# Kernel tuning notes

Hardware: AMD Instinct MI355X
Metric: run time of the kernel (lower is better)

## Reference

```python
import jax, jax.numpy as jnp
import numpy as np

C = 256
POOL = 4

def setup_inputs() -> dict:
    key = jax.random.key(0)
    ks = jax.random.split(key, 8)
    B, H, W = 4, 256, 256
    d = C // 8
    x = jax.random.normal(ks[0], (B, C, H, W), dtype=jnp.float32)
    # 1x1 conv weights stored as [out, in] matrices (kernel_size=1)
    s = 1.0 / np.sqrt(C)
    Wq = jax.random.uniform(ks[1], (d, C), jnp.float32, -s, s)
    bq = jax.random.uniform(ks[2], (d,), jnp.float32, -s, s)
    Wk = jax.random.uniform(ks[3], (d, C), jnp.float32, -s, s)
    bk = jax.random.uniform(ks[4], (d,), jnp.float32, -s, s)
    Wv = jax.random.uniform(ks[5], (C, C), jnp.float32, -s, s)
    bv = jax.random.uniform(ks[6], (C,), jnp.float32, -s, s)
    gamma = jax.random.normal(ks[7], (1,), jnp.float32) * 0.1
    return {"x": x, "Wq": Wq, "bq": bq, "Wk": Wk, "bk": bk,
            "Wv": Wv, "bv": bv, "gamma": gamma}


def reference(x, Wq, bq, Wk, bk, Wv, bv, gamma):
    B, Cc, H, W = x.shape
    Hp, Wp = H // POOL, W // POOL
    # AvgPool2d(kernel=4, stride=4)
    xp = x.reshape(B, Cc, Hp, POOL, Wp, POOL).mean(axis=(3, 5))  # [B,C,Hp,Wp]
    xf = xp.reshape(B, Cc, Hp * Wp)                              # [B,C,N]
    # 1x1 convs == channel matmuls
    q = jnp.einsum('dc,bcn->bdn', Wq, xf) + bq[None, :, None]    # [B,d,N]
    k = jnp.einsum('dc,bcn->bdn', Wk, xf) + bk[None, :, None]    # [B,d,N]
    v = jnp.einsum('ec,bcn->ben', Wv, xf) + bv[None, :, None]    # [B,C,N]
    # energy[b,n,m] = q[:, :, n] . k[:, :, m]
    energy = jnp.einsum('bdn,bdm->bnm', q, k)                    # [B,N,N]
    attn = jax.nn.softmax(energy, axis=-1)
    # out = v @ attn^T  -> out[b,c,n] = sum_m v[b,c,m] * attn[b,n,m]
    out = jnp.einsum('bcm,bnm->bcn', v, attn)                    # [B,C,N]
    out = out.reshape(B, Cc, Hp, Wp)
    # bilinear upsample, half-pixel centers (align_corners=False)
    up = jax.image.resize(out, (B, Cc, H, W), method='bilinear')
    return gamma[0] * up + x
```

## Files before the change

### kernel.cpp

```cpp
#include <hip/hip_runtime.h>

#define B_ 4
#define C_ 256
#define N_ 4096
#define D_ 32

typedef __bf16 bf16;
typedef __bf16 bf16x4 __attribute__((ext_vector_type(4)));
typedef __bf16 bf16x8 __attribute__((ext_vector_type(8)));
typedef float f32x4 __attribute__((ext_vector_type(4)));

__global__ __launch_bounds__(256) void k_prep(
    const float* __restrict__ Wq, const float* __restrict__ bq,
    const float* __restrict__ Wk, const float* __restrict__ bk,
    const float* __restrict__ Wv, const float* __restrict__ bv,
    bf16* __restrict__ wt, float* __restrict__ bias) {
  int r = blockIdx.x, t = threadIdx.x;
  const float* src; float bval;
  if (r < 32)      { src = Wq + (r << 8);        bval = bq[r]; }
  else if (r < 64) { src = Wk + ((r - 32) << 8); bval = bk[r - 32]; }
  else             { src = Wv + ((r - 64) << 8); bval = bv[r - 64]; }
  wt[(r << 8) + t] = (bf16)src[t];
  if (t == 0) bias[r] = bval;
}

__global__ __launch_bounds__(1024) void k_fused(const float* __restrict__ x,
    const bf16* __restrict__ wt, const float* __restrict__ bias,
    bf16* __restrict__ qt, bf16* __restrict__ kt, bf16* __restrict__ v) {
  __shared__ bf16 xsb[64][264];
  int tid = threadIdx.x, wave = tid >> 6, l = tid & 63;
  int lg = l >> 4, ll = l & 15;
  int b = blockIdx.x >> 6, hp = blockIdx.x & 63, n0 = hp * 64;

  const float4* x4 = reinterpret_cast<const float4*>(x) +
      ((size_t)((b * 256 + wave * 16) * 256 + hp * 4)) * 64 + l;
  for (int c0 = 0; c0 < 16; c0 += 4) {
    float s[4] = {0.f, 0.f, 0.f, 0.f};
    #pragma unroll
    for (int j = 0; j < 4; ++j) {
      const float4* p = x4 + (size_t)(c0 + j) * 16384;
      #pragma unroll
      for (int dh = 0; dh < 4; ++dh) {
        float4 a = p[dh * 64];
        s[j] += a.x + a.y + a.z + a.w;
      }
    }
    bf16x4 pk;
    #pragma unroll
    for (int j = 0; j < 4; ++j) pk[j] = (bf16)(s[j] * 0.0625f);
    *reinterpret_cast<bf16x4*>(&xsb[l][wave * 16 + c0]) = pk;
  }
  __syncthreads();

  f32x4 acc[2][4];
  #pragma unroll
  for (int j = 0; j < 2; ++j)
    #pragma unroll
    for (int cb = 0; cb < 4; ++cb) acc[j][cb] = (f32x4){0.f, 0.f, 0.f, 0.f};

  for (int kk = 0; kk < 8; ++kk) {
    bf16x8 bfr[4];
    #pragma unroll
    for (int cb = 0; cb < 4; ++cb)
      bfr[cb] = *reinterpret_cast<const bf16x8*>(&xsb[cb * 16 + ll][kk * 32 + lg * 8]);
    #pragma unroll
    for (int j = 0; j < 2; ++j) {
      int rb = wave + j * 16;
      if (rb < 20) {
        bf16x8 afr = *reinterpret_cast<const bf16x8*>(
            wt + ((size_t)(rb * 16 + ll)) * 256 + kk * 32 + lg * 8);
        #pragma unroll
        for (int cb = 0; cb < 4; ++cb)
          acc[j][cb] = __builtin_amdgcn_mfma_f32_16x16x32_bf16(afr, bfr[cb], acc[j][cb], 0, 0, 0);
      }
    }
  }

  #pragma unroll
  for (int j = 0; j < 2; ++j) {
    int rb = wave + j * 16;
    if (rb < 20) {
      int row0 = rb * 16 + lg * 4;
      float4 b4 = *reinterpret_cast<const float4*>(bias + row0);
      #pragma unroll
      for (int cb = 0; cb < 4; ++cb) {
        int n = n0 + cb * 16 + ll;
        float v0 = acc[j][cb][0] + b4.x, v1 = acc[j][cb][1] + b4.y;
        float v2 = acc[j][cb][2] + b4.z, v3 = acc[j][cb][3] + b4.w;
        if (row0 < 32) {
          bf16x4 pk = {(bf16)v0, (bf16)v1, (bf16)v2, (bf16)v3};
          *reinterpret_cast<bf16x4*>(qt + ((size_t)(b * N_ + n)) * D_ + row0) = pk;
        } else if (row0 < 64) {
          bf16x4 pk = {(bf16)v0, (bf16)v1, (bf16)v2, (bf16)v3};
          *reinterpret_cast<bf16x4*>(kt + ((size_t)(b * N_ + n)) * D_ + row0 - 32) = pk;
        } else {
          int c = row0 - 64;
          v[((size_t)(b * 256 + c + 0)) * N_ + n] = (bf16)v0;
          v[((size_t)(b * 256 + c + 1)) * N_ + n] = (bf16)v1;
          v[((size_t)(b * 256 + c + 2)) * N_ + n] = (bf16)v2;
          v[((size_t)(b * 256 + c + 3)) * N_ + n] = (bf16)v3;
        }
      }
    }
  }
}

__global__ __launch_bounds__(1024) void k_attn(const bf16* __restrict__ qt,
    const bf16* __restrict__ kt, const bf16* __restrict__ v,
    float* __restrict__ outs) {
  __shared__ bf16 p_s[2][64][256];
  __shared__ float l_red[16][64];
  __shared__ float l_s[64];
  int tid = threadIdx.x, wave = tid >> 6, l = tid & 63;
  int lg = l >> 4, ll = l & 15;
  int blk = blockIdx.x;
  int b  = (blk & 7) >> 1;
  int nt = ((blk >> 3) << 1) | (blk & 1);
  int n0 = nt * 64;

  const f32x4 fz = {0.f, 0.f, 0.f, 0.f};

  bf16x8 aq[4];
  #pragma unroll
  for (int tnf = 0; tnf < 4; ++tnf)
    aq[tnf] = *reinterpret_cast<const bf16x8*>(
        qt + ((size_t)(b * N_ + n0 + tnf * 16 + ll)) * D_ + lg * 8);

  f32x4 acc[4];
  float lsum[4];
  #pragma unroll
  for (int a = 0; a < 4; ++a) { acc[a] = fz; lsum[a] = 0.f; }

  const int mw = wave * 16;
  const int colw = mw + ll;
  const bf16* vbase = v + ((size_t)(b << 8)) * N_;

  const int st_blk = 2 * wave + (lg >> 1);
  const int st_el  = (lg & 1) * 4;

  {
    bf16x8 bk8 = *reinterpret_cast<const bf16x8*>(
        kt + ((size_t)(b * N_ + colw)) * D_ + lg * 8);
    #pragma unroll
    for (int tnf = 0; tnf < 4; ++tnf) {
      f32x4 e = __builtin_amdgcn_mfma_f32_16x16x32_bf16(bk8, aq[tnf], fz, 0, 0, 0);
      int row = tnf * 16 + ll;
      bf16x4 pk;
      #pragma unroll
      for (int r = 0; r < 4; ++r) {
        float p = __expf(e[r]);
        lsum[tnf] += p;
        pk[r] = (bf16)p;
      }
      int col = ((st_blk ^ (row & 7)) << 3) + st_el;
      *reinterpret_cast<bf16x4*>(&p_s[0][row][col]) = pk;
    }
  }
  __syncthreads();

  for (int t = 0; t < 15; ++t) {
    int m0 = t * 256;
    int cur = t & 1, nxt = cur ^ 1;
    bf16x8 bk8 = *reinterpret_cast<const bf16x8*>(
        kt + ((size_t)(b * N_ + m0 + 256 + colw)) * D_ + lg * 8);
    #pragma unroll
    for (int kk = 0; kk < 8; ++kk) {
      bf16x8 bv8 = *reinterpret_cast<const bf16x8*>(
          vbase + ((size_t)colw) * N_ + m0 + kk * 32 + lg * 8);
      #pragma unroll
      for (int tnf = 0; tnf < 4; ++tnf) {
        int row = tnf * 16 + ll;
        int col = (((kk * 4 + lg) ^ (ll & 7)) << 3);
        bf16x8 pa = *reinterpret_cast<const bf16x8*>(&p_s[cur][row][col]);
        acc[tnf] = __builtin_amdgcn_mfma_f32_16x16x32_bf16(pa, bv8, acc[tnf], 0, 0, 0);
      }
    }
    #pragma unroll
    for (int tnf = 0; tnf < 4; ++tnf) {
      f32x4 e = __builtin_amdgcn_mfma_f32_16x16x32_bf16(bk8, aq[tnf], fz, 0, 0, 0);
      int row = tnf * 16 + ll;
      bf16x4 pk;
      #pragma unroll
      for (int r = 0; r < 4; ++r) {
        float p = __expf(e[r]);
        lsum[tnf] += p;
        pk[r] = (bf16)p;
      }
      int col = ((st_blk ^ (row & 7)) << 3) + st_el;
      *reinterpret_cast<bf16x4*>(&p_s[nxt][row][col]) = pk;
    }
    __syncthreads();
  }
  {
    int m0 = 15 * 256;
    #pragma unroll
    for (int kk = 0; kk < 8; ++kk) {
      bf16x8 bv8 = *reinterpret_cast<const bf16x8*>(
          vbase + ((size_t)colw) * N_ + m0 + kk * 32 + lg * 8);
      #pragma unroll
      for (int tnf = 0; tnf < 4; ++tnf) {
        int row = tnf * 16 + ll;
        int col = (((kk * 4 + lg) ^ (ll & 7)) << 3);
        bf16x8 pa = *reinterpret_cast<const bf16x8*>(&p_s[1][row][col]);
        acc[tnf] = __builtin_amdgcn_mfma_f32_16x16x32_bf16(pa, bv8, acc[tnf], 0, 0, 0);
      }
    }
  }

  #pragma unroll
  for (int tnf = 0; tnf < 4; ++tnf) {
    float s = lsum[tnf];
    s += __shfl_xor(s, 16);
    s += __shfl_xor(s, 32);
    if (l < 16) l_red[wave][tnf * 16 + l] = s;
  }
  __syncthreads();
  if (tid < 64) {
    float s = 0.f;
    #pragma unroll
    for (int w = 0; w < 16; ++w) s += l_red[w][tid];
    l_s[tid] = s;
  }
  __syncthreads();

  #pragma unroll
  for (int tnf = 0; tnf < 4; ++tnf) {
    int tn0 = tnf * 16 + lg * 4;
    float4 o;
    o.x = acc[tnf][0] / l_s[tn0 + 0];
    o.y = acc[tnf][1] / l_s[tn0 + 1];
    o.z = acc[tnf][2] / l_s[tn0 + 2];
    o.w = acc[tnf][3] / l_s[tn0 + 3];
    *reinterpret_cast<float4*>(outs + ((size_t)((b << 8) + colw)) * N_ + n0 + tn0) = o;
  }
}

__global__ __launch_bounds__(256) void k_up(const float* __restrict__ outs,
    const float* __restrict__ x, const float* __restrict__ gamma,
    float* __restrict__ out) {
  __shared__ float s_o[4096];
  int tid = threadIdx.x, wave = tid >> 6, tw = tid & 63;
  int bc = blockIdx.x;
  const float* src = outs + (size_t)bc * 4096;
  #pragma unroll
  for (int ch = 0; ch < 4; ++ch)
    *reinterpret_cast<float4*>(&s_o[ch * 1024 + tid * 4]) =
        *reinterpret_cast<const float4*>(src + ch * 1024 + tid * 4);
  __syncthreads();

  float g = gamma[0];
  const float4* xr = reinterpret_cast<const float4*>(x) + (size_t)bc * 16384;
  float4* outr = reinterpret_cast<float4*>(out) + (size_t)bc * 16384;

  int twm = tw == 0 ? 0 : tw - 1;
  int twp = tw == 63 ? 63 : tw + 1;

  for (int hb = 0; hb < 64; ++hb) {
    int h = hb * 4 + wave;
    int th = 2 * h - 3;
    int h0 = th < 0 ? -1 : (th >> 3);
    float fh = (float)(th - 8 * h0) * 0.125f;
    int i0h = h0 < 0 ? 0 : h0;
    int i1h = h0 + 1 > 63 ? 63 : h0 + 1;
    const float* r0 = &s_o[i0h * 64];
    const float* r1 = &s_o[i1h * 64];
    float a_m = r0[twm], a_c = r0[tw], a_p = r0[twp];
    float b_m = r1[twm], b_c = r1[tw], b_p = r1[twp];
    float t0 = a_m + 0.625f * (a_c - a_m), u0 = b_m + 0.625f * (b_c - b_m);
    float t1 = a_m + 0.875f * (a_c - a_m), u1 = b_m + 0.875f * (b_c - b_m);
    float t2 = a_c + 0.125f * (a_p - a_c), u2 = b_c + 0.125f * (b_p - b_c);
    float t3 = a_c + 0.375f * (a_p - a_c), u3 = b_c + 0.375f * (b_p - b_c);
    float4 xv = xr[h * 64 + tw];
    float4 o;
    o.x = g * (t0 + fh * (u0 - t0)) + xv.x;
    o.y = g * (t1 + fh * (u1 - t1)) + xv.y;
    o.z = g * (t2 + fh * (u2 - t2)) + xv.z;
    o.w = g * (t3 + fh * (u3 - t3)) + xv.w;
    outr[h * 64 + tw] = o;
  }
}

extern "C" void kernel_launch(void* const* d_in, const int* in_sizes, int n_in,
                              void* d_out, int out_size, void* d_ws, size_t ws_size,
                              hipStream_t stream) {
  const float* x     = (const float*)d_in[0];
  const float* Wq    = (const float*)d_in[1];
  const float* bq    = (const float*)d_in[2];
  const float* Wk    = (const float*)d_in[3];
  const float* bk    = (const float*)d_in[4];
  const float* Wv    = (const float*)d_in[5];
  const float* bv    = (const float*)d_in[6];
  const float* gamma = (const float*)d_in[7];
  float* out = (float*)d_out;

  char* ws = (char*)d_ws;
  float* outs = (float*)(ws);
  bf16*  v    = (bf16*) (ws + (16u << 20));
  bf16*  qt   = (bf16*) (ws + (24u << 20));
  bf16*  kt   = (bf16*) (ws + (25u << 20));
  bf16*  wt   = (bf16*) (ws + (26u << 20));
  float* bias = (float*)(ws + (27u << 20));

  hipLaunchKernelGGL(k_prep,  dim3(320),  dim3(256),  0, stream,
                     Wq, bq, Wk, bk, Wv, bv, wt, bias);
  hipLaunchKernelGGL(k_fused, dim3(256),  dim3(1024), 0, stream,
                     x, wt, bias, qt, kt, v);
  hipLaunchKernelGGL(k_attn,  dim3(256),  dim3(1024), 0, stream, qt, kt, v, outs);
  hipLaunchKernelGGL(k_up,    dim3(1024), dim3(256),  0, stream, outs, x, gamma, out);
}
```

Before: 248.2 us.

## Switch PV accumulation to 32x32x16 MFMA with retiled wave mapping

The P·V product moves from four 16x16x32 bf16 MFMAs per k-step to one 32x32x16 MFMA per 16-column step. Each wave now owns a 32-row by 32-channel output tile (rows split by wave>>3, channels by wave&7) instead of 64 rows by 16 channels. The LDS swizzle for P changes from an XOR over row&7 to one over row&31 to match the new read pattern, and the output store is remapped to the 32x32 accumulator layout. The intent is fewer MFMA issues and fewer LDS reads of P per wave. In exchange, each wave loads V for 32 channels from global memory, which changes global access and reuse.

Measured after the change: 303.9 us. 1.22x slower.

```diff
diff --git a/kernel.cpp b/kernel.cpp
--- a/kernel.cpp
+++ b/kernel.cpp
@@ -9,6 +9,7 @@
 typedef __bf16 bf16x4 __attribute__((ext_vector_type(4)));
 typedef __bf16 bf16x8 __attribute__((ext_vector_type(8)));
 typedef float f32x4 __attribute__((ext_vector_type(4)));
+typedef float f32x16 __attribute__((ext_vector_type(16)));
 
 __global__ __launch_bounds__(256) void k_prep(
     const float* __restrict__ Wq, const float* __restrict__ bq,
@@ -126,17 +127,22 @@
     aq[tnf] = *reinterpret_cast<const bf16x8*>(
         qt + ((size_t)(b * N_ + n0 + tnf * 16 + ll)) * D_ + lg * 8);
 
-  f32x4 acc[4];
+  f32x16 acc;
+  #pragma unroll
+  for (int r = 0; r < 16; ++r) acc[r] = 0.f;
   float lsum[4];
   #pragma unroll
-  for (int a = 0; a < 4; ++a) { acc[a] = fz; lsum[a] = 0.f; }
+  for (int a = 0; a < 4; ++a) lsum[a] = 0.f;
 
   const int mw = wave * 16;
   const int colw = mw + ll;
+  const int nh = wave >> 3;
+  const int cw = (wave & 7) * 32;
+  const int l31 = l & 31, l5 = l >> 5;
   const bf16* vbase = v + ((size_t)(b << 8)) * N_;
 
-  const int st_blk = 2 * wave + (lg >> 1);
-  const int st_el  = (lg & 1) * 4;
+  const int st_g  = 2 * wave + (lg >> 1);
+  const int st_el = (lg & 1) * 4;
 
   {
     bf16x8 bk8 = *reinterpret_cast<const bf16x8*>(
@@ -152,7 +158,7 @@
         lsum[tnf] += p;
         pk[r] = (bf16)p;
       }
-      int col = ((st_blk ^ (row & 7)) << 3) + st_el;
+      int col = ((st_g ^ (row & 31)) << 3) + st_el;
       *reinterpret_cast<bf16x4*>(&p_s[0][row][col]) = pk;
     }
   }
@@ -164,16 +170,13 @@
     bf16x8 bk8 = *reinterpret_cast<const bf16x8*>(
         kt + ((size_t)(b * N_ + m0 + 256 + colw)) * D_ + lg * 8);
     #pragma unroll
-    for (int kk = 0; kk < 8; ++kk) {
+    for (int mi = 0; mi < 16; ++mi) {
       bf16x8 bv8 = *reinterpret_cast<const bf16x8*>(
-          vbase + ((size_t)colw) * N_ + m0 + kk * 32 + lg * 8);
-      #pragma unroll
-      for (int tnf = 0; tnf < 4; ++tnf) {
-        int row = tnf * 16 + ll;
-        int col = (((kk * 4 + lg) ^ (ll & 7)) << 3);
-        bf16x8 pa = *reinterpret_cast<const bf16x8*>(&p_s[cur][row][col]);
-        acc[tnf] = __builtin_amdgcn_mfma_f32_16x16x32_bf16(pa, bv8, acc[tnf], 0, 0, 0);
-      }
+          vbase + ((size_t)(cw + l31)) * N_ + m0 + mi * 16 + l5 * 8);
+      int row = nh * 32 + l31;
+      int col = (((2 * mi + l5) ^ l31) << 3);
+      bf16x8 pa = *reinterpret_cast<const bf16x8*>(&p_s[cur][row][col]);
+      acc = __builtin_amdgcn_mfma_f32_32x32x16_bf16(pa, bv8, acc, 0, 0, 0);
     }
     #pragma unroll
     for (int tnf = 0; tnf < 4; ++tnf) {
@@ -186,7 +189,7 @@
         lsum[tnf] += p;
         pk[r] = (bf16)p;
       }
-      int col = ((st_blk ^ (row & 7)) << 3) + st_el;
+      int col = ((st_g ^ (row & 31)) << 3) + st_el;
       *reinterpret_cast<bf16x4*>(&p_s[nxt][row][col]) = pk;
     }
     __syncthreads();
@@ -194,16 +197,13 @@
   {
     int m0 = 15 * 256;
     #pragma unroll
-    for (int kk = 0; kk < 8; ++kk) {
+    for (int mi = 0; mi < 16; ++mi) {
       bf16x8 bv8 = *reinterpret_cast<const bf16x8*>(
-          vbase + ((size_t)colw) * N_ + m0 + kk * 32 + lg * 8);
-      #pragma unroll
-      for (int tnf = 0; tnf < 4; ++tnf) {
-        int row = tnf * 16 + ll;
-        int col = (((kk * 4 + lg) ^ (ll & 7)) << 3);
-        bf16x8 pa = *reinterpret_cast<const bf16x8*>(&p_s[1][row][col]);
-        acc[tnf] = __builtin_amdgcn_mfma_f32_16x16x32_bf16(pa, bv8, acc[tnf], 0, 0, 0);
-      }
+          vbase + ((size_t)(cw + l31)) * N_ + m0 + mi * 16 + l5 * 8);
+      int row = nh * 32 + l31;
+      int col = (((2 * mi + l5) ^ l31) << 3);
+      bf16x8 pa = *reinterpret_cast<const bf16x8*>(&p_s[1][row][col]);
+      acc = __builtin_amdgcn_mfma_f32_32x32x16_bf16(pa, bv8, acc, 0, 0, 0);
     }
   }
 
@@ -223,15 +223,19 @@
   }
   __syncthreads();
 
-  #pragma unroll
-  for (int tnf = 0; tnf < 4; ++tnf) {
-    int tn0 = tnf * 16 + lg * 4;
-    float4 o;
-    o.x = acc[tnf][0] / l_s[tn0 + 0];
-    o.y = acc[tnf][1] / l_s[tn0 + 1];
-    o.z = acc[tnf][2] / l_s[tn0 + 2];
-    o.w = acc[tnf][3] / l_s[tn0 + 3];
-    *reinterpret_cast<float4*>(outs + ((size_t)((b << 8) + colw)) * N_ + n0 + tn0) = o;
+  {
+    int c = cw + l31;
+    float* orow = outs + ((size_t)((b << 8) + c)) * N_ + n0;
+    #pragma unroll
+    for (int q = 0; q < 4; ++q) {
+      int nb = nh * 32 + 8 * q + 4 * l5;
+      float4 o;
+      o.x = acc[4 * q + 0] / l_s[nb + 0];
+      o.y = acc[4 * q + 1] / l_s[nb + 1];
+      o.z = acc[4 * q + 2] / l_s[nb + 2];
+      o.w = acc[4 * q + 3] / l_s[nb + 3];
+      *reinterpret_cast<float4*>(orow + nb) = o;
+    }
   }
 }
 
```
